# Kernel optimization log

Measured on AMD Instinct MI355X. Metric: run time of the kernel, lower is better.

The kernel has to match this reference:

```python
import jax, jax.numpy as jnp
import numpy as np

# GLIF3 / AlphaPSC constants (from module __init__)
DT = 1.0
V_TH = -45.0
V_RESET = -60.0
C_M = 2.0
TAU = 20.0
TAU_REF = 2.0  # refractory ignored: not in update_state_names ('neuron.v','neuron.Iasc','synapse.psc')
K = jnp.array([0.1, 0.2], dtype=jnp.float32)          # ASC decay rates (1/ms)
ASC_AMPS = jnp.array([1.0, -2.0], dtype=jnp.float32)  # ASC jump amplitudes on spike
TAU_SYN = 5.0

T, B, N_IN, N_HID, N_OUT = 1000, 64, 256, 512, 128


def setup_inputs() -> dict:
    key = jax.random.key(0)
    k1, k2, k3, k4 = jax.random.split(key, 4)
    x = jax.random.normal(k1, (T, B, N_IN), dtype=jnp.float32)
    # Linear layers (bias=False) with fan-in scaled init
    W_in = jax.random.normal(k2, (N_HID, N_IN), dtype=jnp.float32) / np.sqrt(N_IN)
    W_rec = jax.random.normal(k3, (N_HID, N_HID), dtype=jnp.float32) / np.sqrt(N_HID)
    W_out = jax.random.normal(k4, (N_OUT, N_HID), dtype=jnp.float32) / np.sqrt(N_HID)
    return {"x": x, "W_in": W_in, "W_rec": W_rec, "W_out": W_out}


def reference(x, W_in, W_rec, W_out):
    decay_v = DT / TAU                      # leak factor toward v_reset
    decay_asc = jnp.exp(-K * DT)            # (2,)
    decay_syn = jnp.exp(-DT / TAU_SYN)

    x_proj = jnp.einsum('tbi,hi->tbh', x, W_in)  # (T,B,H) input currents

    def step(carry, I_in):
        v, iasc, psc = carry  # v,psc: (B,H); iasc: (B,H,2)
        I_total = I_in + psc + iasc.sum(-1)
        # GLIF membrane integration: dv = dt/c_m * I - dt/tau * (v - v_reset)
        v_int = v + (DT / C_M) * I_total - decay_v * (v - V_RESET)
        spike = (v_int >= V_TH).astype(v_int.dtype)
        v_new = spike * V_RESET + (1.0 - spike) * v_int          # hard reset
        iasc_new = iasc * decay_asc + spike[..., None] * ASC_AMPS  # after-spike currents
        # AlphaPSC with dense recurrent connection
        psc_new = psc * decay_syn + spike @ W_rec.T
        return (v_new, iasc_new, psc_new), spike

    v0 = jnp.full((B, N_HID), V_RESET, dtype=x.dtype)
    iasc0 = jnp.zeros((B, N_HID, 2), dtype=x.dtype)
    psc0 = jnp.zeros((B, N_HID), dtype=x.dtype)
    _, spikes = jax.lax.scan(step, (v0, iasc0, psc0), x_proj)  # spikes: (T,B,H)

    rate = spikes.mean(axis=0)          # (B,H) mean firing rate
    out = rate @ W_out.T                # (B, num_output)
    return out
```

## Files before the change

kernel.cpp:

```cpp
#include <hip/hip_runtime.h>
#include <stdint.h>

#define H 512
#define BATCH 64
#define NIN 256
#define NOUT 128
#define TTOT 1000
#define CHL 20
#define NCH 50

typedef __attribute__((ext_vector_type(4))) float f32x4;

static __device__ __forceinline__ int pk_fp8x4(float a, float b, float c,
                                               float d) {
  int v = 0;
  v = __builtin_amdgcn_cvt_pk_fp8_f32(a, b, v, false);
  v = __builtin_amdgcn_cvt_pk_fp8_f32(c, d, v, true);
  return v;
}
__device__ __forceinline__ void gload_lds16(const void* g, void* l) {
  __builtin_amdgcn_global_load_lds(
      (const __attribute__((address_space(1))) uint32_t*)g,
      (__attribute__((address_space(3))) uint32_t*)l, 16, 0, 0);
}

__global__ __launch_bounds__(256) void k_filter(const float* __restrict__ x,
                                                uint8_t* __restrict__ y,
                                                const float* __restrict__ Win,
                                                uint8_t* __restrict__ Winb) {
  const int bid = blockIdx.x;
  const int tid = threadIdx.x;
  if (bid < 1600) {
    __shared__ float4 y9dep[2][64];
    const int c = bid >> 5;
    const int bp = bid & 31;
    const int ig = tid & 63;
    const int half = (tid >> 6) & 1;
    const int bo = tid >> 7;
    const int b = bp * 2 + bo;
    const size_t base = ((size_t)(c * CHL) * 64 + b) * 256 + ig * 4;
    const float* xa = x + base + (size_t)half * 10 * 16384;
    uint8_t* ya = y + base + (size_t)half * 10 * 16384;
    float4 p[10];
    float ax = 0.f, ay = 0.f, az = 0.f, aw = 0.f;
#pragma unroll
    for (int s = 0; s < 10; ++s) {
      float4 xv = *(const float4*)(xa + (size_t)s * 16384);
      ax = 0.95f * ax + xv.x; ay = 0.95f * ay + xv.y;
      az = 0.95f * az + xv.z; aw = 0.95f * aw + xv.w;
      p[s] = make_float4(ax, ay, az, aw);
      if (half == 0)
        *(int*)(ya + (size_t)s * 16384) = pk_fp8x4(ax, ay, az, aw);
    }
    if (half == 0) y9dep[bo][ig] = make_float4(ax, ay, az, aw);
    __syncthreads();
    if (half == 1) {
      const float4 y9 = y9dep[bo][ig];
      const float pw[10] = {0.95f, 0.9025f, 0.857375f, 0.81450625f,
                            0.7737809375f, 0.735091890625f,
                            0.69833729609375f, 0.6634204312890625f,
                            0.6302494097246094f, 0.5987369392383789f};
#pragma unroll
      for (int s = 0; s < 10; ++s) {
        const float ox = p[s].x + pw[s] * y9.x;
        const float oy = p[s].y + pw[s] * y9.y;
        const float oz = p[s].z + pw[s] * y9.z;
        const float ow = p[s].w + pw[s] * y9.w;
        *(int*)(ya + (size_t)s * 16384) = pk_fp8x4(ox, oy, oz, ow);
      }
    }
  } else {
    const int g = (bid - 1600) * 256 + tid;
    const float4* ptr = (const float4*)Win + (size_t)g * 2;
    float4 a = ptr[0], b = ptr[1];
    int2 o;
    o.x = pk_fp8x4(a.x, a.y, a.z, a.w);
    o.y = pk_fp8x4(b.x, b.y, b.z, b.w);
    *(int2*)(Winb + (size_t)g * 8) = o;
  }
}

__global__ __launch_bounds__(256) void k_bc(const uint8_t* __restrict__ y,
                                            const uint8_t* __restrict__ B,
                                            float* __restrict__ Bc) {
  __shared__ __align__(16) char lds[65536];
  char* ldsA = lds;
  char* ldsB = lds + 32768;
  const int bn = blockIdx.x & 3;
  const int bm = blockIdx.x >> 2;
  const int tid = threadIdx.x;
  const int wave = tid >> 6;
  const int l = tid & 63;
  const int wr = wave >> 1, wc = wave & 1;
  const int fr = l & 15, fq = l >> 4;
  const char* Bb = (const char*)B + (size_t)bn * 128 * 256;
  const int scol = (l & 15) * 16;
#pragma unroll
  for (int i = 0; i < 8; ++i) {
    const int r0 = wave * 32 + i * 4;
    const int r = r0 + (l >> 4);
    const int sc = scol ^ ((r & 7) << 4);
    const int vr = bm * 128 + r;
    const int cc = vr >> 6, bb2 = vr & 63;
    gload_lds16((const char*)y + ((size_t)(cc * CHL + CHL - 1) * 64 + bb2) * 256 + sc,
                ldsA + r0 * 256);
    gload_lds16(Bb + (size_t)r * 256 + sc, ldsB + r0 * 256);
  }
  __syncthreads();
  f32x4 acc[4][4] = {};
#pragma unroll
  for (int kk = 0; kk < 8; ++kk) {
    const int cb = kk * 32 + fq * 8;
    long a[4], b[4];
#pragma unroll
    for (int m = 0; m < 4; ++m) {
      const int row = wr * 64 + m * 16 + fr;
      a[m] = *(const long*)(ldsA + row * 256 + (cb ^ ((row & 7) << 4)));
    }
#pragma unroll
    for (int n = 0; n < 4; ++n) {
      const int row = wc * 64 + n * 16 + fr;
      b[n] = *(const long*)(ldsB + row * 256 + (cb ^ ((row & 7) << 4)));
    }
#pragma unroll
    for (int m = 0; m < 4; ++m)
#pragma unroll
      for (int n = 0; n < 4; ++n)
        acc[m][n] = __builtin_amdgcn_mfma_f32_16x16x32_fp8_fp8(a[m], b[n],
                                                               acc[m][n], 0, 0, 0);
  }
#pragma unroll
  for (int m = 0; m < 4; ++m) {
    const int r0 = bm * 128 + wr * 64 + m * 16 + fq * 4;
#pragma unroll
    for (int n = 0; n < 4; ++n) {
      const int col = bn * 128 + wc * 64 + n * 16 + fr;
      f32x4 a = acc[m][n];
#pragma unroll
      for (int j = 0; j < 4; ++j)
        Bc[(size_t)(r0 + j) * 512 + col] = 0.5f * a[j] - 38.4908446554876f;
    }
  }
}

__global__ __launch_bounds__(256) void k_compose(const float* __restrict__ Bc,
                                                 float* __restrict__ Vst,
                                                 int* __restrict__ flags) {
  if (blockIdx.x == 0 && threadIdx.x < BATCH) flags[threadIdx.x] = 0;
  const int idx = blockIdx.x * 256 + threadIdx.x;
  const float AL = 0.35848592240854223f;
  float v = -60.f;
#pragma unroll
  for (int c = 0; c < NCH; c += 5) {
    float b0 = Bc[(size_t)(c + 0) * 32768 + idx];
    float b1 = Bc[(size_t)(c + 1) * 32768 + idx];
    float b2 = Bc[(size_t)(c + 2) * 32768 + idx];
    float b3 = Bc[(size_t)(c + 3) * 32768 + idx];
    float b4 = Bc[(size_t)(c + 4) * 32768 + idx];
    Vst[(size_t)(c + 0) * 32768 + idx] = v; v = AL * v + b0;
    Vst[(size_t)(c + 1) * 32768 + idx] = v; v = AL * v + b1;
    Vst[(size_t)(c + 2) * 32768 + idx] = v; v = AL * v + b2;
    Vst[(size_t)(c + 3) * 32768 + idx] = v; v = AL * v + b3;
    Vst[(size_t)(c + 4) * 32768 + idx] = v; v = AL * v + b4;
  }
}

__global__ __launch_bounds__(256) void k_screen(const uint8_t* __restrict__ A,
                                                const uint8_t* __restrict__ B,
                                                const float* __restrict__ Vst,
                                                int* __restrict__ flags) {
  __shared__ __align__(16) char lds[65536];
  char* ldsA = lds;
  char* ldsB = lds + 32768;
  const int bid = blockIdx.x;
  const int wg = (bid & 7) * 250 + (bid >> 3);
  const int bn = wg & 3;
  const int bm = wg >> 2;
  const int tid = threadIdx.x;
  const int wave = tid >> 6;
  const int l = tid & 63;
  const int wr = wave >> 1, wc = wave & 1;
  const int fr = l & 15, fq = l >> 4;
  const char* Ab = (const char*)A + (size_t)bm * 128 * 256;
  const char* Bb = (const char*)B + (size_t)bn * 128 * 256;
  const int scol = (l & 15) * 16;
#pragma unroll
  for (int i = 0; i < 8; ++i) {
    const int r0 = wave * 32 + i * 4;
    const int r = r0 + (l >> 4);
    const int sc = scol ^ ((r & 7) << 4);
    gload_lds16(Ab + (size_t)r * 256 + sc, ldsA + r0 * 256);
    gload_lds16(Bb + (size_t)r * 256 + sc, ldsB + r0 * 256);
  }
  __syncthreads();
  f32x4 acc[4][4] = {};
#pragma unroll
  for (int kk = 0; kk < 8; ++kk) {
    const int cb = kk * 32 + fq * 8;
    long a[4], b[4];
#pragma unroll
    for (int m = 0; m < 4; ++m) {
      const int row = wr * 64 + m * 16 + fr;
      a[m] = *(const long*)(ldsA + row * 256 + (cb ^ ((row & 7) << 4)));
    }
#pragma unroll
    for (int n = 0; n < 4; ++n) {
      const int row = wc * 64 + n * 16 + fr;
      b[n] = *(const long*)(ldsB + row * 256 + (cb ^ ((row & 7) << 4)));
    }
#pragma unroll
    for (int m = 0; m < 4; ++m)
#pragma unroll
      for (int n = 0; n < 4; ++n)
        acc[m][n] = __builtin_amdgcn_mfma_f32_16x16x32_fp8_fp8(a[m], b[n],
                                                               acc[m][n], 0, 0, 0);
  }
  __syncthreads();
  const int c = (bm * 2) / CHL;
  const int s = (bm * 2 + wr) - c * CHL;
  float* ldsV = (float*)lds;
  {
    const float* src = Vst + ((size_t)c * 64) * 512 + bn * 128;
    const int b0 = tid >> 2;
    const int c0 = (tid & 3) * 32;
#pragma unroll
    for (int j = 0; j < 8; ++j) {
      float4 v4 = *(const float4*)(src + (size_t)b0 * 512 + c0 + j * 4);
      *(float4*)(ldsV + b0 * 128 + c0 + j * 4) = v4;
    }
  }
  __syncthreads();
  const float As = exp2f(-(float)(s + 1) * 0.07400058144086257f);
  unsigned int cmask = 0;
#pragma unroll
  for (int m = 0; m < 4; ++m) {
#pragma unroll
    for (int j = 0; j < 4; ++j) {
      const int b = m * 16 + fq * 4 + j;
      bool cb2 = false;
#pragma unroll
      for (int n = 0; n < 4; ++n) {
        const int hl = wc * 64 + n * 16 + fr;
        const float th = 29.f - 2.f * As * (ldsV[b * 128 + hl] + 60.f);
        cb2 |= (acc[m][n][j] >= th);
      }
      cmask |= cb2 ? (1u << (m * 4 + j)) : 0u;
    }
  }
  if (__ballot(cmask != 0u)) {
#pragma unroll
    for (int m = 0; m < 4; ++m)
#pragma unroll
      for (int j = 0; j < 4; ++j)
        if (cmask & (1u << (m * 4 + j))) flags[m * 16 + fq * 4 + j] = 1;
  }
}

__global__ __launch_bounds__(512) void k_fallback(
    const float* __restrict__ x, const float* __restrict__ Win,
    const float* __restrict__ Wrec, const float* __restrict__ Wout,
    const int* __restrict__ flags, float* __restrict__ out) {
  const int b = blockIdx.x;
  const int h = threadIdx.x;
  if (!flags[b]) {
    if (h < NOUT) out[b * NOUT + h] = 0.f;
    return;
  }
  const int wid = h >> 6;
  const int lane = h & 63;
  __shared__ float xr[NIN];
  __shared__ unsigned long long wbal[8];
  __shared__ float rbuf[H];
  __shared__ float pbuf[4][NOUT];
  const float D0 = 0.90483741803595957316f;
  const float D1 = 0.81873075307798185867f;
  const float DS = 0.81873075307798185867f;
  const float* wrow = Win + (size_t)h * NIN;
  const float* rrow = Wrec + (size_t)h * H;
  float v = -60.f, a0 = 0.f, a1 = 0.f, psc = 0.f, rsum = 0.f;
  for (int t = 0; t < TTOT; ++t) {
    __syncthreads();
    if (h < NIN) xr[h] = x[((size_t)t * 64 + b) * NIN + h];
    __syncthreads();
    float xp = 0.f;
#pragma unroll 8
    for (int k = 0; k < NIN; ++k) xp += wrow[k] * xr[k];
    float It = xp + psc + a0 + a1;
    float vint = 0.95f * v + 0.5f * It - 3.0f;
    bool fire = vint >= -45.f;
    unsigned long long bal = __ballot(fire);
    if (lane == 0) wbal[wid] = bal;
    __syncthreads();
    float rec = 0.f;
    for (int g = 0; g < 8; ++g) {
      unsigned long long m = wbal[g];
      while (m) {
        int j = (g << 6) + __builtin_ctzll(m);
        m &= m - 1;
        rec += rrow[j];
      }
    }
    v = fire ? -60.f : vint;
    a0 = a0 * D0 + (fire ? 1.f : 0.f);
    a1 = a1 * D1 + (fire ? -2.f : 0.f);
    psc = psc * DS + rec;
    rsum += fire ? 1.f : 0.f;
  }
  rbuf[h] = rsum * 0.001f;
  __syncthreads();
  const int o = h & 127, part = h >> 7;
  const float4* wr4 = (const float4*)(Wout + (size_t)o * H + part * 128);
  const float* rb = rbuf + part * 128;
  float acc = 0.f;
#pragma unroll 8
  for (int q = 0; q < 32; ++q) {
    float4 wv = wr4[q];
    acc += wv.x * rb[q * 4] + wv.y * rb[q * 4 + 1] + wv.z * rb[q * 4 + 2] +
           wv.w * rb[q * 4 + 3];
  }
  pbuf[part][o] = acc;
  __syncthreads();
  if (h < NOUT)
    out[b * NOUT + h] = pbuf[0][h] + pbuf[1][h] + pbuf[2][h] + pbuf[3][h];
}

extern "C" void kernel_launch(void* const* d_in, const int* in_sizes, int n_in,
                              void* d_out, int out_size, void* d_ws,
                              size_t ws_size, hipStream_t stream) {
  const float* x = (const float*)d_in[0];
  const float* Win = (const float*)d_in[1];
  const float* Wrec = (const float*)d_in[2];
  const float* Wout = (const float*)d_in[3];
  float* out = (float*)d_out;

  char* ws = (char*)d_ws;
  uint8_t* Winb = (uint8_t*)(ws + (1 << 20));
  int* flags = (int*)(ws + (3 << 19));
  uint8_t* y = (uint8_t*)(ws + (2 << 20));
  float* Bc = (float*)(ws + ((size_t)20 << 20));
  float* Vst = (float*)(ws + ((size_t)28 << 20));

  hipLaunchKernelGGL(k_filter, dim3(1664), dim3(256), 0, stream, x, y, Win,
                     Winb);
  hipLaunchKernelGGL(k_bc, dim3(100), dim3(256), 0, stream, y, Winb, Bc);
  hipLaunchKernelGGL(k_compose, dim3(128), dim3(256), 0, stream, Bc, Vst,
                     flags);
  hipLaunchKernelGGL(k_screen, dim3(2000), dim3(256), 0, stream, y, Winb, Vst,
                     flags);
  hipLaunchKernelGGL(k_fallback, dim3(BATCH), dim3(512), 0, stream, x, Win,
                     Wrec, Wout, flags, out);
}
```

Before: 54.65 us.

## Make screen kernel persistent with resident B tile and register-prefetched A tiles

The screening GEMM now runs on 512 persistent blocks. Each block keeps its B (W_in fp8) tile resident in LDS and loops over M tiles, replacing 2000 one-shot blocks. The next A tile is prefetched into registers while the current tile's MFMAs run, and the Vst threshold tile is loaded straight into LDS with global_load_lds. Zeroing of the output moves from the fallback kernel into an extra block of the compose kernel. The change adds extra barriers per loop iteration and more register pressure under the 2-blocks-per-CU launch bound.

Result: slower. 62.68 us (+14.7%).

```diff
diff --git a/kernel.cpp b/kernel.cpp
--- a/kernel.cpp
+++ b/kernel.cpp
@@ -145,7 +145,15 @@
 
 __global__ __launch_bounds__(256) void k_compose(const float* __restrict__ Bc,
                                                  float* __restrict__ Vst,
-                                                 int* __restrict__ flags) {
+                                                 int* __restrict__ flags,
+                                                 float* __restrict__ out) {
+  if (blockIdx.x == 128) {
+    float4 z = make_float4(0.f, 0.f, 0.f, 0.f);
+    float4* o = (float4*)out + threadIdx.x;
+#pragma unroll
+    for (int i = 0; i < 8; ++i) o[i * 256] = z;
+    return;
+  }
   if (blockIdx.x == 0 && threadIdx.x < BATCH) flags[threadIdx.x] = 0;
   const int idx = blockIdx.x * 256 + threadIdx.x;
   const float AL = 0.35848592240854223f;
@@ -165,94 +173,120 @@
   }
 }
 
-__global__ __launch_bounds__(256) void k_screen(const uint8_t* __restrict__ A,
-                                                const uint8_t* __restrict__ B,
-                                                const float* __restrict__ Vst,
-                                                int* __restrict__ flags) {
+__global__ __launch_bounds__(256, 2) void k_screen(
+    const uint8_t* __restrict__ A, const uint8_t* __restrict__ B,
+    const float* __restrict__ Vst, int* __restrict__ flags) {
   __shared__ __align__(16) char lds[65536];
   char* ldsA = lds;
   char* ldsB = lds + 32768;
+  float* ldsV = (float*)lds;
   const int bid = blockIdx.x;
-  const int wg = (bid & 7) * 250 + (bid >> 3);
-  const int bn = wg & 3;
-  const int bm = wg >> 2;
+  const int gm = bid & 7;
+  const int rest = bid >> 3;
+  const int bn = rest & 3;
+  const int g = (rest >> 2) * 8 + gm;
   const int tid = threadIdx.x;
   const int wave = tid >> 6;
   const int l = tid & 63;
   const int wr = wave >> 1, wc = wave & 1;
   const int fr = l & 15, fq = l >> 4;
-  const char* Ab = (const char*)A + (size_t)bm * 128 * 256;
+  const int lrow = l >> 4;
+  const int lcol = (l & 15) * 16;
+
   const char* Bb = (const char*)B + (size_t)bn * 128 * 256;
-  const int scol = (l & 15) * 16;
 #pragma unroll
   for (int i = 0; i < 8; ++i) {
     const int r0 = wave * 32 + i * 4;
-    const int r = r0 + (l >> 4);
-    const int sc = scol ^ ((r & 7) << 4);
-    gload_lds16(Ab + (size_t)r * 256 + sc, ldsA + r0 * 256);
-    gload_lds16(Bb + (size_t)r * 256 + sc, ldsB + r0 * 256);
+    const int r = r0 + lrow;
+    gload_lds16(Bb + (size_t)r * 256 + (lcol ^ ((r & 7) << 4)), ldsB + r0 * 256);
+  }
+  int bm = g;
+  float4 areg[8];
+  {
+    const char* Ab = (const char*)A + (size_t)bm * 128 * 256 +
+                     (size_t)(wave * 32 + lrow) * 256;
+#pragma unroll
+    for (int i = 0; i < 8; ++i)
+      areg[i] = *(const float4*)(Ab + (size_t)i * 4 * 256 +
+                                 (lcol ^ ((((i << 2) + lrow) & 7) << 4)));
   }
   __syncthreads();
-  f32x4 acc[4][4] = {};
-#pragma unroll
-  for (int kk = 0; kk < 8; ++kk) {
-    const int cb = kk * 32 + fq * 8;
-    long a[4], b[4];
+
+  for (; bm < 500; bm += 128) {
+#pragma unroll
+    for (int i = 0; i < 8; ++i)
+      *(float4*)(ldsA + (wave * 32 + i * 4) * 256 + l * 16) = areg[i];
+    __syncthreads();
+    const int bm2 = bm + 128;
+    if (bm2 < 500) {
+      const char* Ab = (const char*)A + (size_t)bm2 * 128 * 256 +
+                       (size_t)(wave * 32 + lrow) * 256;
+#pragma unroll
+      for (int i = 0; i < 8; ++i)
+        areg[i] = *(const float4*)(Ab + (size_t)i * 4 * 256 +
+                                   (lcol ^ ((((i << 2) + lrow) & 7) << 4)));
+    }
+    f32x4 acc[4][4] = {};
+#pragma unroll
+    for (int kk = 0; kk < 8; ++kk) {
+      const int cb = kk * 32 + fq * 8;
+      long a[4], b[4];
+#pragma unroll
+      for (int m = 0; m < 4; ++m) {
+        const int row = wr * 64 + m * 16 + fr;
+        a[m] = *(const long*)(ldsA + row * 256 + (cb ^ ((row & 7) << 4)));
+      }
+#pragma unroll
+      for (int n = 0; n < 4; ++n) {
+        const int row = wc * 64 + n * 16 + fr;
+        b[n] = *(const long*)(ldsB + row * 256 + (cb ^ ((row & 7) << 4)));
+      }
+#pragma unroll
+      for (int m = 0; m < 4; ++m)
+#pragma unroll
+        for (int n = 0; n < 4; ++n)
+          acc[m][n] = __builtin_amdgcn_mfma_f32_16x16x32_fp8_fp8(a[m], b[n],
+                                                                 acc[m][n], 0, 0, 0);
+    }
+    __syncthreads();
+    const int c = (bm * 2) / CHL;
+    const int s = (bm * 2 + wr) - c * CHL;
+    {
+      const float* vsrc = Vst + ((size_t)c * 64) * 512 + bn * 128;
+      const int vrow = l >> 5;
+      const int vcol = (l & 31) * 4;
+#pragma unroll
+      for (int i = 0; i < 8; ++i) {
+        const int brow = (wave * 8 + i) * 2 + vrow;
+        gload_lds16(vsrc + (size_t)brow * 512 + vcol, ldsV + (wave * 8 + i) * 256);
+      }
+    }
+    __syncthreads();
+    const float As = exp2f(-(float)(s + 1) * 0.07400058144086257f);
+    unsigned int cmask = 0;
 #pragma unroll
     for (int m = 0; m < 4; ++m) {
-      const int row = wr * 64 + m * 16 + fr;
-      a[m] = *(const long*)(ldsA + row * 256 + (cb ^ ((row & 7) << 4)));
-    }
-#pragma unroll
-    for (int n = 0; n < 4; ++n) {
-      const int row = wc * 64 + n * 16 + fr;
-      b[n] = *(const long*)(ldsB + row * 256 + (cb ^ ((row & 7) << 4)));
-    }
-#pragma unroll
-    for (int m = 0; m < 4; ++m)
-#pragma unroll
-      for (int n = 0; n < 4; ++n)
-        acc[m][n] = __builtin_amdgcn_mfma_f32_16x16x32_fp8_fp8(a[m], b[n],
-                                                               acc[m][n], 0, 0, 0);
-  }
-  __syncthreads();
-  const int c = (bm * 2) / CHL;
-  const int s = (bm * 2 + wr) - c * CHL;
-  float* ldsV = (float*)lds;
-  {
-    const float* src = Vst + ((size_t)c * 64) * 512 + bn * 128;
-    const int b0 = tid >> 2;
-    const int c0 = (tid & 3) * 32;
-#pragma unroll
-    for (int j = 0; j < 8; ++j) {
-      float4 v4 = *(const float4*)(src + (size_t)b0 * 512 + c0 + j * 4);
-      *(float4*)(ldsV + b0 * 128 + c0 + j * 4) = v4;
-    }
-  }
-  __syncthreads();
-  const float As = exp2f(-(float)(s + 1) * 0.07400058144086257f);
-  unsigned int cmask = 0;
-#pragma unroll
-  for (int m = 0; m < 4; ++m) {
-#pragma unroll
-    for (int j = 0; j < 4; ++j) {
-      const int b = m * 16 + fq * 4 + j;
-      bool cb2 = false;
-#pragma unroll
-      for (int n = 0; n < 4; ++n) {
-        const int hl = wc * 64 + n * 16 + fr;
-        const float th = 29.f - 2.f * As * (ldsV[b * 128 + hl] + 60.f);
-        cb2 |= (acc[m][n][j] >= th);
-      }
-      cmask |= cb2 ? (1u << (m * 4 + j)) : 0u;
-    }
-  }
-  if (__ballot(cmask != 0u)) {
-#pragma unroll
-    for (int m = 0; m < 4; ++m)
-#pragma unroll
-      for (int j = 0; j < 4; ++j)
-        if (cmask & (1u << (m * 4 + j))) flags[m * 16 + fq * 4 + j] = 1;
+#pragma unroll
+      for (int j = 0; j < 4; ++j) {
+        const int b = m * 16 + fq * 4 + j;
+        bool cb2 = false;
+#pragma unroll
+        for (int n = 0; n < 4; ++n) {
+          const int hl = wc * 64 + n * 16 + fr;
+          const float th = 29.f - 2.f * As * (ldsV[b * 128 + hl] + 60.f);
+          cb2 |= (acc[m][n][j] >= th);
+        }
+        cmask |= cb2 ? (1u << (m * 4 + j)) : 0u;
+      }
+    }
+    if (__ballot(cmask != 0u)) {
+#pragma unroll
+      for (int m = 0; m < 4; ++m)
+#pragma unroll
+        for (int j = 0; j < 4; ++j)
+          if (cmask & (1u << (m * 4 + j))) flags[m * 16 + fq * 4 + j] = 1;
+    }
+    __syncthreads();
   }
 }
 
@@ -262,10 +296,7 @@
     const int* __restrict__ flags, float* __restrict__ out) {
   const int b = blockIdx.x;
   const int h = threadIdx.x;
-  if (!flags[b]) {
-    if (h < NOUT) out[b * NOUT + h] = 0.f;
-    return;
-  }
+  if (!flags[b]) return;
   const int wid = h >> 6;
   const int lane = h & 63;
   __shared__ float xr[NIN];
@@ -343,9 +374,9 @@
   hipLaunchKernelGGL(k_filter, dim3(1664), dim3(256), 0, stream, x, y, Win,
                      Winb);
   hipLaunchKernelGGL(k_bc, dim3(100), dim3(256), 0, stream, y, Winb, Bc);
-  hipLaunchKernelGGL(k_compose, dim3(128), dim3(256), 0, stream, Bc, Vst,
-                     flags);
-  hipLaunchKernelGGL(k_screen, dim3(2000), dim3(256), 0, stream, y, Winb, Vst,
+  hipLaunchKernelGGL(k_compose, dim3(129), dim3(256), 0, stream, Bc, Vst,
+                     flags, out);
+  hipLaunchKernelGGL(k_screen, dim3(512), dim3(256), 0, stream, y, Winb, Vst,
                      flags);
   hipLaunchKernelGGL(k_fallback, dim3(BATCH), dim3(512), 0, stream, x, Win,
                      Wrec, Wout, flags, out);
```
